# Kernel optimization log

Measured on AMD Instinct MI355X. Metric: run time of the kernel, lower is better.

Reference implementation:

```python
import jax, jax.numpy as jnp
import numpy as np

NUM_WIRES = 20
DEPTH = 4


def setup_inputs() -> dict:
    key = jax.random.key(0)
    x = jax.random.normal(key, (NUM_WIRES,), dtype=jnp.float32)
    return {"x": x}


def _apply_1q(state, gate, wire):
    # state: flat [2^n] complex; apply 2x2 gate on `wire`
    s = state.reshape(2 ** wire, 2, -1)
    return jnp.einsum('ab,ibj->iaj', gate, s).reshape(-1)


def _apply_cnot(state, control):
    # CNOT on adjacent wires (control, control+1): flip target where control==1
    s = state.reshape(2 ** control, 2, 2, -1)
    s = jnp.concatenate([s[:, :1], s[:, 1:, ::-1]], axis=1)
    return s.reshape(-1)


def _simulate(x):
    n = NUM_WIRES
    state = jnp.zeros(2 ** n, dtype=jnp.complex64).at[0].set(1.0)
    half = (x.astype(jnp.float32) * 0.5)
    c = jnp.cos(half).astype(jnp.complex64)  # [n]
    s = jnp.sin(half).astype(jnp.complex64)  # [n]
    for _ in range(DEPTH):
        for w in range(n):
            cw, sw = c[w], s[w]
            rx = jnp.stack([jnp.stack([cw, -1j * sw]), jnp.stack([-1j * sw, cw])])
            ry = jnp.stack([jnp.stack([cw, -sw]), jnp.stack([sw, cw])])
            state = _apply_1q(state, rx, w)
            state = _apply_1q(state, ry, w)
        for w in range(n - 1):
            state = _apply_cnot(state, w)
    probs = jnp.abs(state) ** 2  # real float32 [2^n]
    expz = []
    for i in range(n):
        p = probs.reshape(2 ** i, 2, -1).sum(axis=(0, 2))
        expz.append(p[0] - p[1])
    return jnp.stack(expz).astype(jnp.float32)  # [n] <Z_i>


def reference(x):
    return _simulate(x)
```

## Files before the change

kernel.cpp:

```cpp
#include <hip/hip_runtime.h>


#define NW 20

__device__ __forceinline__ float2 cmul(float2 a, float2 b) {
    return make_float2(a.x*b.x - a.y*b.y, a.x*b.y + a.y*b.x);
}

__device__ __forceinline__ void apply_gate(float2& a0, float2& a1,
                                           float2 u00, float2 u01,
                                           float2 u10, float2 u11) {
    float2 b0, b1;
    b0.x = u00.x*a0.x - u00.y*a0.y + u01.x*a1.x - u01.y*a1.y;
    b0.y = u00.x*a0.y + u00.y*a0.x + u01.x*a1.y + u01.y*a1.x;
    b1.x = u10.x*a0.x - u10.y*a0.y + u11.x*a1.x - u11.y*a1.y;
    b1.y = u10.x*a0.y + u10.y*a0.x + u11.x*a1.y + u11.y*a1.x;
    a0 = b0; a1 = b1;
}

__device__ __forceinline__ float2 shflx(float2 v, int m) {
    float2 r;
    r.x = __shfl_xor(v.x, m, 64);
    r.y = __shfl_xor(v.y, m, 64);
    return r;
}

template<int A>
__device__ __forceinline__ void gate_regbit(float2 (&amp)[8], const float2* __restrict__ Gw) {
    float2 u00 = Gw[0], u01 = Gw[1], u10 = Gw[2], u11 = Gw[3];
    #pragma unroll
    for (int r = 0; r < 8; r++)
        if (!(r & (1 << A)))
            apply_gate(amp[r], amp[r | (1 << A)], u00, u01, u10, u11);
}

template<int A, int LM>
__device__ __forceinline__ void swap_reg_lane(float2 (&amp)[8], unsigned lane) {
    bool hb = (lane & (unsigned)LM) != 0u;
    #pragma unroll
    for (int r = 0; r < 8; r++) {
        if (!(r & (1 << A))) {
            float2 lo = amp[r], hi = amp[r | (1 << A)];
            float2 xs = hb ? lo : hi;
            float2 ys = shflx(xs, LM);
            amp[r]            = hb ? ys : lo;
            amp[r | (1 << A)] = hb ? hi : ys;
        }
    }
}

__global__ void prep_gates(const float* __restrict__ x, float2* __restrict__ G) {
    int w = threadIdx.x;
    if (w < NW) {
        float h = 0.5f * x[w];
        float c = cosf(h), s = sinf(h);
        float cc = c*c, ss = s*s, cs = c*s;
        G[w*4+0] = make_float2(cc,  ss);
        G[w*4+1] = make_float2(-cs, -cs);
        G[w*4+2] = make_float2(cs,  -cs);
        G[w*4+3] = make_float2(cc,  -ss);
    }
}

template<int MODE>
__global__ __launch_bounds__(512) void stageA(const float2* __restrict__ src,
                                              float2* __restrict__ dst,
                                              const float2* __restrict__ G) {
    __shared__ float2 lds[4096];
    const unsigned t = threadIdx.x;
    const unsigned lane = t & 63u, wv = t >> 6;
    const unsigned H   = blockIdx.x;
    const unsigned Hp  = H ^ (H >> 1);
    const unsigned inj = (H & 1u) << 11;
    const unsigned lb  = (wv << 9) | (lane << 3);
    const unsigned gb  = (lb ^ (lb >> 1)) ^ inj;

    float2 amp[8];
    if (MODE == 1) {
        const float4* q = (const float4*)(src + ((size_t)Hp << 12) + (gb & ~7u));
        float4 q0 = q[0], q1 = q[1], q2 = q[2], q3 = q[3];
        float2 e0 = make_float2(q0.x,q0.y), e1 = make_float2(q0.z,q0.w);
        float2 e2 = make_float2(q1.x,q1.y), e3 = make_float2(q1.z,q1.w);
        float2 e4 = make_float2(q2.x,q2.y), e5 = make_float2(q2.z,q2.w);
        float2 e6 = make_float2(q3.x,q3.y), e7 = make_float2(q3.z,q3.w);
        bool f = (gb & 4u) != 0u;
        amp[0] = f ? e4 : e0;  amp[1] = f ? e5 : e1;
        amp[2] = f ? e7 : e3;  amp[3] = f ? e6 : e2;
        amp[4] = f ? e2 : e6;  amp[5] = f ? e3 : e7;
        amp[6] = f ? e1 : e5;  amp[7] = f ? e0 : e4;
    } else {
        float2 P = make_float2(1.0f, 0.0f);
        #pragma unroll
        for (int b = 12; b <= 19; b++)
            P = cmul(P, G[(19-b)*4 + (int)((Hp >> (b-12)) & 1u)*2]);
        #pragma unroll
        for (int b = 3; b <= 11; b++)
            P = cmul(P, G[(19-b)*4 + (int)((gb >> b) & 1u)*2]);
        float2 Tt[8];
        #pragma unroll
        for (int j = 0; j < 8; j++) {
            float2 v = cmul(G[18*4 + ((j>>1)&1)*2], G[19*4 + (j&1)*2]);
            v = cmul(G[17*4 + ((j>>2)&1)*2], v);
            Tt[j] = cmul(P, v);
        }
        bool f = (gb & 4u) != 0u;
        amp[0] = f ? Tt[4] : Tt[0];  amp[1] = f ? Tt[5] : Tt[1];
        amp[2] = f ? Tt[7] : Tt[3];  amp[3] = f ? Tt[6] : Tt[2];
        amp[4] = f ? Tt[2] : Tt[6];  amp[5] = f ? Tt[3] : Tt[7];
        amp[6] = f ? Tt[1] : Tt[5];  amp[7] = f ? Tt[0] : Tt[4];
    }

    gate_regbit<0>(amp, G + 19*4);
    gate_regbit<1>(amp, G + 18*4);
    gate_regbit<2>(amp, G + 17*4);
    swap_reg_lane<0,1>(amp, lane);
    swap_reg_lane<1,2>(amp, lane);
    swap_reg_lane<2,4>(amp, lane);
    gate_regbit<0>(amp, G + 16*4);
    gate_regbit<1>(amp, G + 15*4);
    gate_regbit<2>(amp, G + 14*4);
    swap_reg_lane<0,8>(amp, lane);
    swap_reg_lane<1,16>(amp, lane);
    swap_reg_lane<2,32>(amp, lane);
    gate_regbit<0>(amp, G + 13*4);
    gate_regbit<1>(amp, G + 12*4);
    gate_regbit<2>(amp, G + 11*4);
    #pragma unroll
    for (int k = 0; k < 8; k++) lds[(wv << 9) | ((unsigned)k << 6) | lane] = amp[k];
    __syncthreads();
    #pragma unroll
    for (int k = 0; k < 8; k++) amp[k] = lds[((unsigned)k << 9) | (wv << 6) | lane];
    gate_regbit<0>(amp, G + 10*4);
    gate_regbit<1>(amp, G +  9*4);
    gate_regbit<2>(amp, G +  8*4);
    float2* d = dst + ((size_t)H << 12);
    #pragma unroll
    for (int k = 0; k < 8; k++) d[((unsigned)k << 9) | (wv << 6) | lane] = amp[k];
}

template<int FUSE>
__global__ __launch_bounds__(512) void stageB(float2* __restrict__ st,
                                              const float2* __restrict__ G,
                                              float* __restrict__ partial) {
    __shared__ float2 lds[4096];
    const unsigned t = threadIdx.x, lane = t & 63u, wv = t >> 6;
    const unsigned bb = blockIdx.x;
    const unsigned m = lane & 15u, l45 = lane >> 4;

    float2 amp[8];
    #pragma unroll
    for (int k = 0; k < 8; k++) {
        unsigned h = (unsigned)k | (l45 << 3) | (wv << 5);
        amp[k] = st[((size_t)h << 12) | (bb << 4) | m];
    }
    gate_regbit<0>(amp, G + 7*4);
    gate_regbit<1>(amp, G + 6*4);
    gate_regbit<2>(amp, G + 5*4);
    swap_reg_lane<0,16>(amp, lane);
    swap_reg_lane<1,32>(amp, lane);
    gate_regbit<0>(amp, G + 4*4);
    gate_regbit<1>(amp, G + 3*4);
    #pragma unroll
    for (int k = 0; k < 8; k++) {
        unsigned li = lane | ((((unsigned)k >> 2) & 1u) << 6) | (((unsigned)k & 1u) << 7)
                    | ((((unsigned)k >> 1) & 1u) << 8) | (wv << 9);
        lds[li] = amp[k];
    }
    __syncthreads();
    #pragma unroll
    for (int k = 0; k < 8; k++) amp[k] = lds[lane | (wv << 6) | ((unsigned)k << 9)];
    gate_regbit<0>(amp, G + 2*4);
    gate_regbit<1>(amp, G + 1*4);
    gate_regbit<2>(amp, G + 0*4);

    if (!FUSE) {
        #pragma unroll
        for (int k = 0; k < 8; k++) {
            unsigned h = l45 | (wv << 2) | ((unsigned)k << 5);
            st[((size_t)h << 12) | (bb << 4) | m] = amp[k];
        }
    } else {
        float p[8];
        #pragma unroll
        for (int k = 0; k < 8; k++) p[k] = amp[k].x*amp[k].x + amp[k].y*amp[k].y;
        float Se = p[0]+p[3]+p[5]+p[6];
        float So = p[1]+p[2]+p[4]+p[7];
        float D  = Se - So;
        float S0 = (p[0]+p[1]+p[2]+p[3]) - (p[4]+p[5]+p[6]+p[7]);
        float S1 = (p[0]+p[1]+p[6]+p[7]) - (p[2]+p[3]+p[4]+p[5]);
        unsigned hlow = l45 | (wv << 2);
        unsigned v = (hlow << 12) | (bb << 4) | m;
        unsigned cm = v; cm ^= cm >> 1; cm ^= cm >> 2; cm ^= cm >> 4;
        cm ^= cm >> 8; cm ^= cm >> 16;
        float acc[NW];
        acc[0] = S0; acc[1] = S1; acc[2] = D;
        #pragma unroll
        for (int w = 3; w < NW; w++)
            acc[w] = ((cm >> (19 - w)) & 1u) ? -D : D;

        __syncthreads();
        float* red = (float*)lds;
        #pragma unroll
        for (int w = 0; w < NW; w++) {
            float s = acc[w];
            #pragma unroll
            for (int off = 32; off; off >>= 1) s += __shfl_down(s, off, 64);
            if (lane == 0) red[wv*NW + w] = s;
        }
        __syncthreads();
        if (t < NW) {
            float s = 0.0f;
            #pragma unroll
            for (int w8 = 0; w8 < 8; w8++) s += red[w8*NW + (int)t];
            partial[bb*NW + t] = s;
        }
    }
}

__global__ __launch_bounds__(256) void reduce_out(const float* __restrict__ partial,
                                                  float* __restrict__ out) {
    __shared__ float red[4*NW];
    unsigned t = threadIdx.x;
    float vals[NW];
    #pragma unroll
    for (int w = 0; w < NW; w++) vals[w] = partial[t*NW + w];
    #pragma unroll
    for (int w = 0; w < NW; w++) {
        float v = vals[w];
        #pragma unroll
        for (int off = 32; off; off >>= 1) v += __shfl_down(v, off, 64);
        if ((t & 63u) == 0u) red[(t >> 6)*NW + w] = v;
    }
    __syncthreads();
    if (t < NW) out[t] = red[t] + red[NW+t] + red[2*NW+t] + red[3*NW+t];
}

extern "C" void kernel_launch(void* const* d_in, const int* in_sizes, int n_in,
                              void* d_out, int out_size, void* d_ws, size_t ws_size,
                              hipStream_t stream) {
    (void)in_sizes; (void)n_in; (void)out_size; (void)ws_size;
    const float* x = (const float*)d_in[0];
    float* out = (float*)d_out;

    char* ws = (char*)d_ws;
    float2* gates   = (float2*)ws;
    float*  partial = (float*)(ws + 1024);
    float2* buf0    = (float2*)(ws + 65536);
    float2* buf1    = (float2*)(ws + 65536 + (size_t)(8u << 20));

    prep_gates<<<1, 32, 0, stream>>>(x, gates);
    stageA<0><<<256, 512, 0, stream>>>(buf1 , buf0, gates);
    stageB<0><<<256, 512, 0, stream>>>(buf0, gates, nullptr);
    stageA<1><<<256, 512, 0, stream>>>(buf0, buf1, gates);
    stageB<0><<<256, 512, 0, stream>>>(buf1, gates, nullptr);
    stageA<1><<<256, 512, 0, stream>>>(buf1, buf0, gates);
    stageB<1><<<256, 512, 0, stream>>>(buf0, gates, partial);
    reduce_out<<<1, 256, 0, stream>>>(partial, out);
}
```

Before: 72.75 us.

## Halve amplitudes per thread with 1024-thread blocks and fold gate prep into stages

Each thread now holds 4 amplitudes instead of 8, and blocks grow to 1024 threads, so every gate pass is restructured. There are more lane-shuffle swaps and an extra LDS transpose round with additional barriers. The separate prep_gates launch is removed: each block computes the gate matrices itself into shared memory. The aim is more parallelism and latency hiding per CU and one fewer kernel launch, at the cost of extra syncs, shuffles and redundant trig per block.

```diff
diff --git a/kernel.cpp b/kernel.cpp
--- a/kernel.cpp
+++ b/kernel.cpp
@@ -25,20 +25,24 @@
     return r;
 }
 
+__device__ __forceinline__ unsigned sfx(unsigned x) {
+    x ^= x >> 1; x ^= x >> 2; x ^= x >> 4; x ^= x >> 8; x ^= x >> 16; return x;
+}
+
 template<int A>
-__device__ __forceinline__ void gate_regbit(float2 (&amp)[8], const float2* __restrict__ Gw) {
+__device__ __forceinline__ void gate_regbit4(float2 (&amp)[4], const float2* Gw) {
     float2 u00 = Gw[0], u01 = Gw[1], u10 = Gw[2], u11 = Gw[3];
     #pragma unroll
-    for (int r = 0; r < 8; r++)
+    for (int r = 0; r < 4; r++)
         if (!(r & (1 << A)))
             apply_gate(amp[r], amp[r | (1 << A)], u00, u01, u10, u11);
 }
 
 template<int A, int LM>
-__device__ __forceinline__ void swap_reg_lane(float2 (&amp)[8], unsigned lane) {
+__device__ __forceinline__ void swap_reg_lane4(float2 (&amp)[4], unsigned lane) {
     bool hb = (lane & (unsigned)LM) != 0u;
     #pragma unroll
-    for (int r = 0; r < 8; r++) {
+    for (int r = 0; r < 4; r++) {
         if (!(r & (1 << A))) {
             float2 lo = amp[r], hi = amp[r | (1 << A)];
             float2 xs = hb ? lo : hi;
@@ -49,153 +53,167 @@
     }
 }
 
-__global__ void prep_gates(const float* __restrict__ x, float2* __restrict__ G) {
-    int w = threadIdx.x;
-    if (w < NW) {
-        float h = 0.5f * x[w];
+__device__ __forceinline__ void prep_Gs(const float* __restrict__ x, float2* Gs,
+                                        unsigned t) {
+    if (t < NW) {
+        float h = 0.5f * x[t];
         float c = cosf(h), s = sinf(h);
         float cc = c*c, ss = s*s, cs = c*s;
-        G[w*4+0] = make_float2(cc,  ss);
-        G[w*4+1] = make_float2(-cs, -cs);
-        G[w*4+2] = make_float2(cs,  -cs);
-        G[w*4+3] = make_float2(cc,  -ss);
+        Gs[t*4+0] = make_float2(cc,  ss);
+        Gs[t*4+1] = make_float2(-cs, -cs);
+        Gs[t*4+2] = make_float2(cs,  -cs);
+        Gs[t*4+3] = make_float2(cc,  -ss);
     }
 }
 
 template<int MODE>
-__global__ __launch_bounds__(512) void stageA(const float2* __restrict__ src,
-                                              float2* __restrict__ dst,
-                                              const float2* __restrict__ G) {
+__global__ __launch_bounds__(1024) void stageA(const float* __restrict__ x,
+                                               const float2* __restrict__ src,
+                                               float2* __restrict__ dst) {
     __shared__ float2 lds[4096];
+    __shared__ float2 Gs[4*NW];
     const unsigned t = threadIdx.x;
+    prep_Gs(x, Gs, t);
+    __syncthreads();
     const unsigned lane = t & 63u, wv = t >> 6;
+    const unsigned w0 = wv & 1u, w1 = (wv >> 1) & 1u, w2 = (wv >> 2) & 1u, w3 = wv >> 3;
     const unsigned H   = blockIdx.x;
     const unsigned Hp  = H ^ (H >> 1);
     const unsigned inj = (H & 1u) << 11;
-    const unsigned lb  = (wv << 9) | (lane << 3);
+    const unsigned lb  = (wv << 8) | (lane << 2);
     const unsigned gb  = (lb ^ (lb >> 1)) ^ inj;
 
-    float2 amp[8];
+    float2 amp[4];
     if (MODE == 1) {
-        const float4* q = (const float4*)(src + ((size_t)Hp << 12) + (gb & ~7u));
-        float4 q0 = q[0], q1 = q[1], q2 = q[2], q3 = q[3];
+        const float4* q = (const float4*)(src + ((size_t)Hp << 12) + (gb & ~3u));
+        float4 q0 = q[0], q1 = q[1];
         float2 e0 = make_float2(q0.x,q0.y), e1 = make_float2(q0.z,q0.w);
         float2 e2 = make_float2(q1.x,q1.y), e3 = make_float2(q1.z,q1.w);
-        float2 e4 = make_float2(q2.x,q2.y), e5 = make_float2(q2.z,q2.w);
-        float2 e6 = make_float2(q3.x,q3.y), e7 = make_float2(q3.z,q3.w);
-        bool f = (gb & 4u) != 0u;
-        amp[0] = f ? e4 : e0;  amp[1] = f ? e5 : e1;
-        amp[2] = f ? e7 : e3;  amp[3] = f ? e6 : e2;
-        amp[4] = f ? e2 : e6;  amp[5] = f ? e3 : e7;
-        amp[6] = f ? e1 : e5;  amp[7] = f ? e0 : e4;
+        bool s2 = (gb & 2u) != 0u;
+        amp[0] = s2 ? e2 : e0;
+        amp[1] = s2 ? e3 : e1;
+        amp[2] = s2 ? e1 : e3;
+        amp[3] = s2 ? e0 : e2;
     } else {
         float2 P = make_float2(1.0f, 0.0f);
         #pragma unroll
         for (int b = 12; b <= 19; b++)
-            P = cmul(P, G[(19-b)*4 + (int)((Hp >> (b-12)) & 1u)*2]);
-        #pragma unroll
-        for (int b = 3; b <= 11; b++)
-            P = cmul(P, G[(19-b)*4 + (int)((gb >> b) & 1u)*2]);
-        float2 Tt[8];
-        #pragma unroll
-        for (int j = 0; j < 8; j++) {
-            float2 v = cmul(G[18*4 + ((j>>1)&1)*2], G[19*4 + (j&1)*2]);
-            v = cmul(G[17*4 + ((j>>2)&1)*2], v);
-            Tt[j] = cmul(P, v);
-        }
-        bool f = (gb & 4u) != 0u;
-        amp[0] = f ? Tt[4] : Tt[0];  amp[1] = f ? Tt[5] : Tt[1];
-        amp[2] = f ? Tt[7] : Tt[3];  amp[3] = f ? Tt[6] : Tt[2];
-        amp[4] = f ? Tt[2] : Tt[6];  amp[5] = f ? Tt[3] : Tt[7];
-        amp[6] = f ? Tt[1] : Tt[5];  amp[7] = f ? Tt[0] : Tt[4];
-    }
-
-    gate_regbit<0>(amp, G + 19*4);
-    gate_regbit<1>(amp, G + 18*4);
-    gate_regbit<2>(amp, G + 17*4);
-    swap_reg_lane<0,1>(amp, lane);
-    swap_reg_lane<1,2>(amp, lane);
-    swap_reg_lane<2,4>(amp, lane);
-    gate_regbit<0>(amp, G + 16*4);
-    gate_regbit<1>(amp, G + 15*4);
-    gate_regbit<2>(amp, G + 14*4);
-    swap_reg_lane<0,8>(amp, lane);
-    swap_reg_lane<1,16>(amp, lane);
-    swap_reg_lane<2,32>(amp, lane);
-    gate_regbit<0>(amp, G + 13*4);
-    gate_regbit<1>(amp, G + 12*4);
-    gate_regbit<2>(amp, G + 11*4);
-    #pragma unroll
-    for (int k = 0; k < 8; k++) lds[(wv << 9) | ((unsigned)k << 6) | lane] = amp[k];
-    __syncthreads();
-    #pragma unroll
-    for (int k = 0; k < 8; k++) amp[k] = lds[((unsigned)k << 9) | (wv << 6) | lane];
-    gate_regbit<0>(amp, G + 10*4);
-    gate_regbit<1>(amp, G +  9*4);
-    gate_regbit<2>(amp, G +  8*4);
+            P = cmul(P, Gs[(19-b)*4 + (int)((Hp >> (b-12)) & 1u)*2]);
+        #pragma unroll
+        for (int b = 2; b <= 11; b++)
+            P = cmul(P, Gs[(19-b)*4 + (int)((gb >> b) & 1u)*2]);
+        float2 T[4];
+        #pragma unroll
+        for (int j = 0; j < 4; j++)
+            T[j] = cmul(P, cmul(Gs[19*4 + (j&1)*2], Gs[18*4 + ((j>>1)&1)*2]));
+        bool s2 = (gb & 2u) != 0u;
+        amp[0] = s2 ? T[2] : T[0];
+        amp[1] = s2 ? T[3] : T[1];
+        amp[2] = s2 ? T[1] : T[3];
+        amp[3] = s2 ? T[0] : T[2];
+    }
+
+    gate_regbit4<0>(amp, Gs + 19*4);
+    gate_regbit4<1>(amp, Gs + 18*4);
+    swap_reg_lane4<0,1>(amp, lane);
+    swap_reg_lane4<1,2>(amp, lane);
+    gate_regbit4<0>(amp, Gs + 17*4);
+    gate_regbit4<1>(amp, Gs + 16*4);
+    swap_reg_lane4<0,4>(amp, lane);
+    swap_reg_lane4<1,8>(amp, lane);
+    gate_regbit4<0>(amp, Gs + 15*4);
+    gate_regbit4<1>(amp, Gs + 14*4);
+    swap_reg_lane4<0,16>(amp, lane);
+    swap_reg_lane4<1,32>(amp, lane);
+    gate_regbit4<0>(amp, Gs + 13*4);
+    gate_regbit4<1>(amp, Gs + 12*4);
+    #pragma unroll
+    for (int k = 0; k < 4; k++) lds[lane | ((unsigned)k << 6) | (wv << 8)] = amp[k];
+    __syncthreads();
+    #pragma unroll
+    for (int k = 0; k < 4; k++)
+        amp[k] = lds[lane | (w0 << 6) | (w1 << 7) | ((unsigned)k << 8) | (w2 << 10) | (w3 << 11)];
+    gate_regbit4<0>(amp, Gs + 11*4);
+    gate_regbit4<1>(amp, Gs + 10*4);
+    __syncthreads();
+    #pragma unroll
+    for (int k = 0; k < 4; k++) lds[lane | ((unsigned)k << 6) | (wv << 8)] = amp[k];
+    __syncthreads();
+    #pragma unroll
+    for (int k = 0; k < 4; k++)
+        amp[k] = lds[lane | (w2 << 6) | (w3 << 7) | (w0 << 8) | (w1 << 9) | ((unsigned)k << 10)];
+    gate_regbit4<0>(amp, Gs + 9*4);
+    gate_regbit4<1>(amp, Gs + 8*4);
     float2* d = dst + ((size_t)H << 12);
     #pragma unroll
-    for (int k = 0; k < 8; k++) d[((unsigned)k << 9) | (wv << 6) | lane] = amp[k];
+    for (int k = 0; k < 4; k++)
+        d[lane | (w0 << 6) | (w1 << 7) | (w2 << 8) | (w3 << 9) | ((unsigned)k << 10)] = amp[k];
 }
 
 template<int FUSE>
-__global__ __launch_bounds__(512) void stageB(float2* __restrict__ st,
-                                              const float2* __restrict__ G,
-                                              float* __restrict__ partial) {
+__global__ __launch_bounds__(1024) void stageB(const float* __restrict__ x,
+                                               float2* __restrict__ st,
+                                               float* __restrict__ partial) {
     __shared__ float2 lds[4096];
-    const unsigned t = threadIdx.x, lane = t & 63u, wv = t >> 6;
+    __shared__ float2 Gs[4*NW];
+    const unsigned t = threadIdx.x;
+    prep_Gs(x, Gs, t);
+    __syncthreads();
+    const unsigned lane = t & 63u, wv = t >> 6;
+    const unsigned w0 = wv & 1u, w1 = (wv >> 1) & 1u, w2 = (wv >> 2) & 1u, w3 = wv >> 3;
     const unsigned bb = blockIdx.x;
-    const unsigned m = lane & 15u, l45 = lane >> 4;
-
-    float2 amp[8];
-    #pragma unroll
-    for (int k = 0; k < 8; k++) {
-        unsigned h = (unsigned)k | (l45 << 3) | (wv << 5);
+    const unsigned m = lane & 15u, l4 = (lane >> 4) & 1u, l5 = lane >> 5;
+
+    float2 amp[4];
+    #pragma unroll
+    for (int k = 0; k < 4; k++) {
+        unsigned h = (unsigned)k | (l4 << 2) | (l5 << 3) | (wv << 4);
         amp[k] = st[((size_t)h << 12) | (bb << 4) | m];
     }
-    gate_regbit<0>(amp, G + 7*4);
-    gate_regbit<1>(amp, G + 6*4);
-    gate_regbit<2>(amp, G + 5*4);
-    swap_reg_lane<0,16>(amp, lane);
-    swap_reg_lane<1,32>(amp, lane);
-    gate_regbit<0>(amp, G + 4*4);
-    gate_regbit<1>(amp, G + 3*4);
-    #pragma unroll
-    for (int k = 0; k < 8; k++) {
-        unsigned li = lane | ((((unsigned)k >> 2) & 1u) << 6) | (((unsigned)k & 1u) << 7)
-                    | ((((unsigned)k >> 1) & 1u) << 8) | (wv << 9);
-        lds[li] = amp[k];
-    }
-    __syncthreads();
-    #pragma unroll
-    for (int k = 0; k < 8; k++) amp[k] = lds[lane | (wv << 6) | ((unsigned)k << 9)];
-    gate_regbit<0>(amp, G + 2*4);
-    gate_regbit<1>(amp, G + 1*4);
-    gate_regbit<2>(amp, G + 0*4);
+    gate_regbit4<0>(amp, Gs + 7*4);
+    gate_regbit4<1>(amp, Gs + 6*4);
+    swap_reg_lane4<0,16>(amp, lane);
+    swap_reg_lane4<1,32>(amp, lane);
+    gate_regbit4<0>(amp, Gs + 5*4);
+    gate_regbit4<1>(amp, Gs + 4*4);
+    #pragma unroll
+    for (int k = 0; k < 4; k++) lds[lane | ((unsigned)k << 6) | (wv << 8)] = amp[k];
+    __syncthreads();
+    #pragma unroll
+    for (int k = 0; k < 4; k++)
+        amp[k] = lds[lane | (w0 << 6) | (w1 << 7) | ((unsigned)k << 8) | (w2 << 10) | (w3 << 11)];
+    gate_regbit4<0>(amp, Gs + 3*4);
+    gate_regbit4<1>(amp, Gs + 2*4);
+    __syncthreads();
+    #pragma unroll
+    for (int k = 0; k < 4; k++) lds[lane | ((unsigned)k << 6) | (wv << 8)] = amp[k];
+    __syncthreads();
+    #pragma unroll
+    for (int k = 0; k < 4; k++)
+        amp[k] = lds[lane | (w2 << 6) | (w3 << 7) | (w0 << 8) | (w1 << 9) | ((unsigned)k << 10)];
+    gate_regbit4<0>(amp, Gs + 1*4);
+    gate_regbit4<1>(amp, Gs + 0*4);
 
     if (!FUSE) {
         #pragma unroll
-        for (int k = 0; k < 8; k++) {
-            unsigned h = l45 | (wv << 2) | ((unsigned)k << 5);
+        for (int k = 0; k < 4; k++) {
+            unsigned h = l4 | (l5 << 1) | (w0 << 2) | (w1 << 3) | (w2 << 4) | (w3 << 5)
+                       | (((unsigned)k & 1u) << 6) | (((unsigned)k >> 1) << 7);
             st[((size_t)h << 12) | (bb << 4) | m] = amp[k];
         }
     } else {
-        float p[8];
-        #pragma unroll
-        for (int k = 0; k < 8; k++) p[k] = amp[k].x*amp[k].x + amp[k].y*amp[k].y;
-        float Se = p[0]+p[3]+p[5]+p[6];
-        float So = p[1]+p[2]+p[4]+p[7];
-        float D  = Se - So;
-        float S0 = (p[0]+p[1]+p[2]+p[3]) - (p[4]+p[5]+p[6]+p[7]);
-        float S1 = (p[0]+p[1]+p[6]+p[7]) - (p[2]+p[3]+p[4]+p[5]);
-        unsigned hlow = l45 | (wv << 2);
-        unsigned v = (hlow << 12) | (bb << 4) | m;
-        unsigned cm = v; cm ^= cm >> 1; cm ^= cm >> 2; cm ^= cm >> 4;
-        cm ^= cm >> 8; cm ^= cm >> 16;
+        float p[4];
+        #pragma unroll
+        for (int k = 0; k < 4; k++) p[k] = amp[k].x*amp[k].x + amp[k].y*amp[k].y;
+        float S19 = (p[0] + p[1]) - (p[2] + p[3]);
+        float D   = p[0] - p[1] - p[2] + p[3];
+        unsigned v = m | (bb << 4) | (l4 << 12) | (l5 << 13) | (w0 << 14)
+                   | (w1 << 15) | (w2 << 16) | (w3 << 17);
+        unsigned cm = sfx(v);
         float acc[NW];
-        acc[0] = S0; acc[1] = S1; acc[2] = D;
-        #pragma unroll
-        for (int w = 3; w < NW; w++)
+        acc[0] = S19; acc[1] = D;
+        #pragma unroll
+        for (int w = 2; w < NW; w++)
             acc[w] = ((cm >> (19 - w)) & 1u) ? -D : D;
 
         __syncthreads();
@@ -211,7 +229,7 @@
         if (t < NW) {
             float s = 0.0f;
             #pragma unroll
-            for (int w8 = 0; w8 < 8; w8++) s += red[w8*NW + (int)t];
+            for (int v16 = 0; v16 < 16; v16++) s += red[v16*NW + (int)t];
             partial[bb*NW + t] = s;
         }
     }
@@ -243,17 +261,15 @@
     float* out = (float*)d_out;
 
     char* ws = (char*)d_ws;
-    float2* gates   = (float2*)ws;
     float*  partial = (float*)(ws + 1024);
     float2* buf0    = (float2*)(ws + 65536);
     float2* buf1    = (float2*)(ws + 65536 + (size_t)(8u << 20));
 
-    prep_gates<<<1, 32, 0, stream>>>(x, gates);
-    stageA<0><<<256, 512, 0, stream>>>(buf1 , buf0, gates);
-    stageB<0><<<256, 512, 0, stream>>>(buf0, gates, nullptr);
-    stageA<1><<<256, 512, 0, stream>>>(buf0, buf1, gates);
-    stageB<0><<<256, 512, 0, stream>>>(buf1, gates, nullptr);
-    stageA<1><<<256, 512, 0, stream>>>(buf1, buf0, gates);
-    stageB<1><<<256, 512, 0, stream>>>(buf0, gates, partial);
+    stageA<0><<<256, 1024, 0, stream>>>(x, buf1 , buf0);
+    stageB<0><<<256, 1024, 0, stream>>>(x, buf0, nullptr);
+    stageA<1><<<256, 1024, 0, stream>>>(x, buf0, buf1);
+    stageB<0><<<256, 1024, 0, stream>>>(x, buf1, nullptr);
+    stageA<1><<<256, 1024, 0, stream>>>(x, buf1, buf0);
+    stageB<1><<<256, 1024, 0, stream>>>(x, buf0, partial);
     reduce_out<<<1, 256, 0, stream>>>(partial, out);
 }
```

Measured after the change: 63.68 us (median of 2 runs). 12.5% less time.
